# Kernel optimization log

Hardware: AMD Instinct MI355X
Metric: run time of the kernel (lower is better)

Reference implementation:

```python
import jax, jax.numpy as jnp
import numpy as np
from jax import lax

SCALE = 2
K_UP = 5
BN_EPS = 1e-5
DN = ('NCHW', 'OIHW', 'NCHW')


def bn_eval(x, gamma, beta):
    # BatchNorm2d in eval mode with running_mean=0, running_var=1
    s = gamma / jnp.sqrt(1.0 + BN_EPS)
    return x * s[None, :, None, None] + beta[None, :, None, None]


def pixel_shuffle(x, r):
    b, C, h, w = x.shape
    c = C // (r * r)
    x = x.reshape(b, c, r, r, h, w)
    x = x.transpose(0, 1, 4, 2, 5, 3)  # b, c, h, r, w, r
    return x.reshape(b, c, h * r, w * r)


def setup_inputs() -> dict:
    key = jax.random.key(0)
    ks = jax.random.split(key, 3)
    b, c, h, w = 4, 128, 64, 64
    c_mid = 64
    return {
        'X': jax.random.normal(ks[0], (b, c, h, w), dtype=jnp.float32),
        'comp_w': jax.random.normal(ks[1], (c_mid, c, 1, 1), dtype=jnp.float32) * 0.05,
        'comp_g': jnp.ones((c_mid,), jnp.float32),
        'comp_b': jnp.zeros((c_mid,), jnp.float32),
        'enc_w': jax.random.normal(ks[2], ((SCALE * K_UP) ** 2, c_mid, 3, 3), dtype=jnp.float32) * 0.05,
        'enc_g': jnp.ones(((SCALE * K_UP) ** 2,), jnp.float32),
        'enc_b': jnp.zeros(((SCALE * K_UP) ** 2,), jnp.float32),
    }


def reference(X, comp_w, comp_g, comp_b, enc_w, enc_g, enc_b):
    b, c, h, w = X.shape
    h_, w_ = h * SCALE, w * SCALE
    pad = K_UP // 2 * SCALE  # = 4

    # comp: 1x1 conv + BN + SiLU
    W = lax.conv_general_dilated(X, comp_w, (1, 1), [(0, 0), (0, 0)], dimension_numbers=DN)
    W = jax.nn.silu(bn_eval(W, comp_g, comp_b))
    # enc: 3x3 conv (pad 1) + BN, no activation
    W = lax.conv_general_dilated(W, enc_w, (1, 1), [(1, 1), (1, 1)], dimension_numbers=DN)
    W = bn_eval(W, enc_g, enc_b)
    # pixel shuffle -> [b, k_up^2, h_, w_], softmax over kernel dim
    W = pixel_shuffle(W, SCALE)
    W = jax.nn.softmax(W, axis=1)

    # nearest-neighbor upsample of X
    Xu = jnp.repeat(jnp.repeat(X, SCALE, axis=2), SCALE, axis=3)  # [b, c, h_, w_]
    # unfold: kernel k_up, dilation=scale, padding=pad (im2col, channel-major)
    P = lax.conv_general_dilated_patches(
        Xu, (K_UP, K_UP), (1, 1), [(pad, pad), (pad, pad)],
        rhs_dilation=(SCALE, SCALE), dimension_numbers=DN)  # [b, c*k^2, h_, w_]
    P = P.reshape(b, c, K_UP * K_UP, h_, w_)

    return jnp.einsum('bkhw,bckhw->bchw', W, P)
```

## Files before the change

### kernel.cpp

```cpp
#include <hip/hip_runtime.h>
#include <hip/hip_bf16.h>
#include <math.h>

#define Bn   4
#define CIN  128
#define Hh   64
#define Ww   64
#define HW   4096
#define CMID 64
#define KOC  100
#define H2   128
#define W2d  128
#define HW2  16384
#define KUP  5
#define BN_EPS 1e-5f
#define CCH  8

typedef __attribute__((ext_vector_type(4)))  short  short4v;
typedef __attribute__((ext_vector_type(8)))  short  short8v;
typedef __attribute__((ext_vector_type(16))) float  float16v;

__device__ __forceinline__ ushort f2bf(float v) {
    __hip_bfloat16 h = __float2bfloat16(v);
    return *(ushort*)&h;
}

__global__ __launch_bounds__(256) void comp_kernel(
    const float* __restrict__ X,
    const float* __restrict__ cw,
    const float* __restrict__ cg,
    const float* __restrict__ cb,
    const float* __restrict__ ew,
    unsigned* __restrict__ W1b,
    ushort* __restrict__ Abf)
{
    int tid = threadIdx.x;
    if (blockIdx.x < 288) {
        int i   = blockIdx.x * 256 + tid;
        int cm  = i & 63;
        int kop = (i >> 6) & 127;
        int tap = i >> 13;
        float v = (kop < KOC) ? ew[((size_t)(kop * CMID + cm)) * 9 + tap] : 0.f;
        Abf[i] = f2bf(v);
    }

    int gt  = blockIdx.x * 256 + tid;
    int pg  = gt & 1023;
    int cog = (gt >> 10) & 31;
    int b   = gt >> 15;
    int pix = pg * 4;
    int co0 = cog * 2;

    const float* xb = X + (size_t)b * CIN * HW + pix;
    float4 acc0 = make_float4(0.f, 0.f, 0.f, 0.f);
    float4 acc1 = make_float4(0.f, 0.f, 0.f, 0.f);

#pragma unroll 4
    for (int ci = 0; ci < CIN; ++ci) {
        float4 xv = *(const float4*)(xb + (size_t)ci * HW);
        float w0 = cw[(size_t)co0 * CIN + ci];
        float w1 = cw[(size_t)(co0 + 1) * CIN + ci];
        acc0.x += xv.x * w0; acc0.y += xv.y * w0; acc0.z += xv.z * w0; acc0.w += xv.w * w0;
        acc1.x += xv.x * w1; acc1.y += xv.y * w1; acc1.z += xv.z * w1; acc1.w += xv.w * w1;
    }

    float inv_s = rsqrtf(1.0f + BN_EPS);
    float s0 = cg[co0] * inv_s,     bb0 = cb[co0];
    float s1 = cg[co0 + 1] * inv_s, bb1 = cb[co0 + 1];
    float r0[4] = {acc0.x, acc0.y, acc0.z, acc0.w};
    float r1[4] = {acc1.x, acc1.y, acc1.z, acc1.w};
#pragma unroll
    for (int i = 0; i < 4; ++i) {
        float v0 = r0[i] * s0 + bb0; v0 = v0 / (1.f + expf(-v0));
        float v1 = r1[i] * s1 + bb1; v1 = v1 / (1.f + expf(-v1));
        unsigned pk = (unsigned)f2bf(v0) | ((unsigned)f2bf(v1) << 16);
        W1b[((size_t)b * HW + pix + i) * 32 + cog] = pk;
    }
}

__global__ __launch_bounds__(256) void enc_kernel(
    const ushort* __restrict__ W1b_us,
    const ushort* __restrict__ Abf,
    float* __restrict__ W2)
{
    __shared__ ushort Bs[3 * 34 * 72];

    int bid   = blockIdx.x;
    int whalf = bid & 1;
    int h     = (bid >> 1) & 63;
    int b     = bid >> 7;
    int w0    = whalf * 32;
    int tid   = threadIdx.x;

    const unsigned* src  = (const unsigned*)W1b_us;
    unsigned*       dstu = (unsigned*)Bs;
    for (int i = tid; i < 3 * 34 * 32; i += 256) {
        int cp = i & 31;
        int t  = i >> 5;
        int wl = t % 34;
        int r  = t / 34;
        int gr = h - 1 + r, gw = w0 - 1 + wl;
        unsigned val = 0u;
        if ((unsigned)gr < 64u && (unsigned)gw < 64u)
            val = src[((size_t)b * HW + gr * 64 + gw) * 32 + cp];
        dstu[(r * 34 + wl) * 36 + cp] = val;
    }
    __syncthreads();

    int lane = tid & 63;
    int wid  = tid >> 6;
    int n    = lane & 31;
    int q    = lane >> 5;

    float16v acc;
#pragma unroll
    for (int i = 0; i < 16; ++i) acc[i] = 0.f;

    const ushort* Arow = Abf + ((size_t)(wid * 32 + n)) * 64 + q * 8;

#pragma unroll
    for (int tap = 0; tap < 9; ++tap) {
        int dy = tap / 3, dx = tap % 3;
        int bbase = ((dy * 34) + n + dx) * 72 + q * 8;
        const ushort* Atap = Arow + (size_t)tap * 128 * 64;
#pragma unroll
        for (int c = 0; c < 4; ++c) {
            short8v a = *(const short8v*)(Atap + c * 16);
            short8v bf = *(const short8v*)(Bs + bbase + c * 16);
            acc = __builtin_amdgcn_mfma_f32_32x32x16_bf16(a, bf, acc, 0, 0, 0);
        }
    }

    int pixn = h * 64 + w0 + n;
    float* Wp = W2 + (size_t)b * KOC * HW + pixn;
#pragma unroll
    for (int reg = 0; reg < 16; ++reg) {
        int row = (reg & 3) + 8 * (reg >> 2) + 4 * q;
        int ko  = wid * 32 + row;
        if (ko < KOC) Wp[(size_t)ko * HW] = acc[reg];
    }
}

__global__ __launch_bounds__(256) void softmax_kernel(
    const float* __restrict__ W2,
    float* __restrict__ Wsm,
    const float* __restrict__ eg,
    const float* __restrict__ eb)
{
    int idx = blockIdx.x * blockDim.x + threadIdx.x;
    int pix = idx & (HW - 1);
    int sub = (idx >> 12) & 3;
    int b   = idx >> 14;

    float inv_s = rsqrtf(1.0f + BN_EPS);
    const float* pi = W2  + (size_t)b * KOC * HW + pix;
    float*       po = Wsm + (size_t)b * KOC * HW + pix;
    float v[25];
    float m = -1e30f;
#pragma unroll
    for (int k = 0; k < 25; ++k) {
        int ko = 4 * k + sub;
        v[k] = pi[(size_t)ko * HW] * (eg[ko] * inv_s) + eb[ko];
        m = fmaxf(m, v[k]);
    }
    float sum = 0.f;
#pragma unroll
    for (int k = 0; k < 25; ++k) {
        v[k] = expf(v[k] - m);
        sum += v[k];
    }
    float inv = 1.f / sum;
#pragma unroll
    for (int k = 0; k < 25; ++k)
        po[(size_t)(4 * k + sub) * HW] = v[k] * inv;
}

__global__ __launch_bounds__(256) void carafe_kernel(
    const float* __restrict__ X,
    const float* __restrict__ Wsm,
    float* __restrict__ out)
{
    int gt = blockIdx.x * blockDim.x + threadIdx.x;
    int w  = gt & 63;
    int h  = (gt >> 6) & 63;
    int b  = (gt >> 12) & 3;
    int chunk = gt >> 14;
    int c0 = chunk * CCH;
    int pix = h * Ww + w;

    float wt[100];
    const float* wpb = Wsm + (size_t)b * KOC * HW + pix;
#pragma unroll
    for (int k = 0; k < 25; ++k) {
        wt[k]      = wpb[(size_t)(4 * k + 0) * HW];
        wt[25 + k] = wpb[(size_t)(4 * k + 1) * HW];
        wt[50 + k] = wpb[(size_t)(4 * k + 2) * HW];
        wt[75 + k] = wpb[(size_t)(4 * k + 3) * HW];
    }

    int off[25];
#pragma unroll
    for (int ki = 0; ki < 5; ++ki) {
#pragma unroll
        for (int kj = 0; kj < 5; ++kj) {
            int k = ki * 5 + kj;
            int r = h + ki - 2, cc = w + kj - 2;
            bool valid = ((unsigned)r < 64u) && ((unsigned)cc < 64u);
            int rc = r < 0 ? 0 : (r > 63 ? 63 : r);
            int cx = cc < 0 ? 0 : (cc > 63 ? 63 : cc);
            off[k] = rc * Ww + cx;
            if (!valid) { wt[k] = 0.f; wt[25+k] = 0.f; wt[50+k] = 0.f; wt[75+k] = 0.f; }
        }
    }

    const float* xp = X + ((size_t)b * CIN + c0) * HW;
    float* o0 = out + ((size_t)b * CIN + c0) * HW2 + (2 * h) * W2d + 2 * w;

    for (int c = 0; c < CCH; ++c) {
        float x[25];
#pragma unroll
        for (int k = 0; k < 25; ++k) x[k] = xp[off[k]];
        float a0 = 0.f, a1 = 0.f, a2 = 0.f, a3 = 0.f;
#pragma unroll
        for (int k = 0; k < 25; ++k) {
            float xv = x[k];
            a0 += wt[k]      * xv;
            a1 += wt[25 + k] * xv;
            a2 += wt[50 + k] * xv;
            a3 += wt[75 + k] * xv;
        }
        *(float2*)o0          = make_float2(a0, a1);
        *(float2*)(o0 + W2d)  = make_float2(a2, a3);
        xp += HW;
        o0 += HW2;
    }
}

extern "C" void kernel_launch(void* const* d_in, const int* in_sizes, int n_in,
                              void* d_out, int out_size, void* d_ws, size_t ws_size,
                              hipStream_t stream)
{
    const float* X  = (const float*)d_in[0];
    const float* cw = (const float*)d_in[1];
    const float* cg = (const float*)d_in[2];
    const float* cb = (const float*)d_in[3];
    const float* ew = (const float*)d_in[4];
    const float* eg = (const float*)d_in[5];
    const float* eb = (const float*)d_in[6];
    float* out = (float*)d_out;

    char* ws = (char*)d_ws;
    unsigned* W1b = (unsigned*)ws;
    ushort*   Abf = (ushort*)(ws + 2097152);
    float*    W2  = (float*)(ws + 2097152 + 147456);
    float*    Wsm = W2 + (size_t)Bn * KOC * HW;

    comp_kernel   <<<512, 256, 0, stream>>>(X, cw, cg, cb, ew, W1b, Abf);
    enc_kernel    <<<512, 256, 0, stream>>>((const ushort*)W1b, Abf, W2);
    softmax_kernel<<<Bn * 4 * HW / 256, 256, 0, stream>>>(W2, Wsm, eg, eb);
    carafe_kernel <<<16 * Bn * HW / 256, 256, 0, stream>>>(X, Wsm, out);
}
```

Baseline: 129.4 us.

## Fuse BN and softmax into enc MFMA epilogue and restage comp weights in LDS

Moves the BN scale and the per-subpixel softmax into the enc kernel epilogue. Max and sum across the 100 output rows are reduced through shared memory across waves, so the separate softmax kernel and its extra write and read of the 100-channel map are removed. The comp kernel is remapped to one output channel per thread, with the 1x1 weights staged in padded LDS, writing bf16 directly. This doubles the comp grid, and every block reloads the full weight matrix into LDS.

```diff
diff --git a/kernel.cpp b/kernel.cpp
--- a/kernel.cpp
+++ b/kernel.cpp
@@ -31,59 +31,66 @@
     const float* __restrict__ cg,
     const float* __restrict__ cb,
     const float* __restrict__ ew,
-    unsigned* __restrict__ W1b,
+    ushort* __restrict__ W1b,
     ushort* __restrict__ Abf)
 {
+    __shared__ float cwS[64 * 129];
+
     int tid = threadIdx.x;
-    if (blockIdx.x < 288) {
-        int i   = blockIdx.x * 256 + tid;
+    int blk = blockIdx.x;
+
+    for (int i = tid; i < 64 * 128; i += 256) {
+        int co_s = i >> 7, ci_s = i & 127;
+        cwS[co_s * 129 + ci_s] = cw[i];
+    }
+
+    if (blk < 288) {
+        int i   = blk * 256 + tid;
         int cm  = i & 63;
         int kop = (i >> 6) & 127;
         int tap = i >> 13;
         float v = (kop < KOC) ? ew[((size_t)(kop * CMID + cm)) * 9 + tap] : 0.f;
         Abf[i] = f2bf(v);
     }
-
-    int gt  = blockIdx.x * 256 + tid;
-    int pg  = gt & 1023;
-    int cog = (gt >> 10) & 31;
-    int b   = gt >> 15;
-    int pix = pg * 4;
-    int co0 = cog * 2;
+    __syncthreads();
+
+    int b   = blk >> 8;
+    int pix = ((blk & 255) << 4) + ((tid >> 6) << 2);
+    int co  = tid & 63;
 
     const float* xb = X + (size_t)b * CIN * HW + pix;
-    float4 acc0 = make_float4(0.f, 0.f, 0.f, 0.f);
-    float4 acc1 = make_float4(0.f, 0.f, 0.f, 0.f);
+    const float* wrow = cwS + co * 129;
+    float a0 = 0.f, a1 = 0.f, a2 = 0.f, a3 = 0.f;
 
 #pragma unroll 4
     for (int ci = 0; ci < CIN; ++ci) {
         float4 xv = *(const float4*)(xb + (size_t)ci * HW);
-        float w0 = cw[(size_t)co0 * CIN + ci];
-        float w1 = cw[(size_t)(co0 + 1) * CIN + ci];
-        acc0.x += xv.x * w0; acc0.y += xv.y * w0; acc0.z += xv.z * w0; acc0.w += xv.w * w0;
-        acc1.x += xv.x * w1; acc1.y += xv.y * w1; acc1.z += xv.z * w1; acc1.w += xv.w * w1;
+        float w = wrow[ci];
+        a0 += xv.x * w; a1 += xv.y * w; a2 += xv.z * w; a3 += xv.w * w;
     }
 
     float inv_s = rsqrtf(1.0f + BN_EPS);
-    float s0 = cg[co0] * inv_s,     bb0 = cb[co0];
-    float s1 = cg[co0 + 1] * inv_s, bb1 = cb[co0 + 1];
-    float r0[4] = {acc0.x, acc0.y, acc0.z, acc0.w};
-    float r1[4] = {acc1.x, acc1.y, acc1.z, acc1.w};
+    float s0 = cg[co] * inv_s, bb0 = cb[co];
+    float r[4] = {a0, a1, a2, a3};
+    ushort* wp = W1b + ((size_t)b * HW + pix) * 64 + co;
 #pragma unroll
     for (int i = 0; i < 4; ++i) {
-        float v0 = r0[i] * s0 + bb0; v0 = v0 / (1.f + expf(-v0));
-        float v1 = r1[i] * s1 + bb1; v1 = v1 / (1.f + expf(-v1));
-        unsigned pk = (unsigned)f2bf(v0) | ((unsigned)f2bf(v1) << 16);
-        W1b[((size_t)b * HW + pix + i) * 32 + cog] = pk;
+        float v = r[i] * s0 + bb0;
+        v = v / (1.f + expf(-v));
+        wp[(size_t)i * 64] = f2bf(v);
     }
 }
 
 __global__ __launch_bounds__(256) void enc_kernel(
     const ushort* __restrict__ W1b_us,
     const ushort* __restrict__ Abf,
-    float* __restrict__ W2)
+    const float* __restrict__ eg,
+    const float* __restrict__ eb,
+    float* __restrict__ Wsm)
 {
     __shared__ ushort Bs[3 * 34 * 72];
+    __shared__ float  redm[4][8][32];
+    __shared__ float  reds[4][8][32];
 
     int bid   = blockIdx.x;
     int whalf = bid & 1;
@@ -131,48 +138,74 @@
         }
     }
 
+    float inv_s = rsqrtf(1.0f + BN_EPS);
+    int   widq  = wid * 2 + q;
+
+    float v[16];
+    float pmax[4] = {-1e30f, -1e30f, -1e30f, -1e30f};
+#pragma unroll
+    for (int g = 0; g < 4; ++g) {
+        int base = wid * 32 + 8 * g + 4 * q;
+        if (base < KOC) {
+            float4 gg = *(const float4*)(eg + base);
+            float4 bb = *(const float4*)(eb + base);
+            float v0 = acc[4*g+0] * (gg.x * inv_s) + bb.x;
+            float v1 = acc[4*g+1] * (gg.y * inv_s) + bb.y;
+            float v2 = acc[4*g+2] * (gg.z * inv_s) + bb.z;
+            float v3 = acc[4*g+3] * (gg.w * inv_s) + bb.w;
+            v[4*g+0] = v0; v[4*g+1] = v1; v[4*g+2] = v2; v[4*g+3] = v3;
+            pmax[0] = fmaxf(pmax[0], v0);
+            pmax[1] = fmaxf(pmax[1], v1);
+            pmax[2] = fmaxf(pmax[2], v2);
+            pmax[3] = fmaxf(pmax[3], v3);
+        } else {
+            v[4*g+0] = -1e30f; v[4*g+1] = -1e30f;
+            v[4*g+2] = -1e30f; v[4*g+3] = -1e30f;
+        }
+    }
+
+#pragma unroll
+    for (int j = 0; j < 4; ++j) redm[j][widq][n] = pmax[j];
+    __syncthreads();
+    float m[4];
+#pragma unroll
+    for (int j = 0; j < 4; ++j) {
+        float mm = redm[j][0][n];
+#pragma unroll
+        for (int i = 1; i < 8; ++i) mm = fmaxf(mm, redm[j][i][n]);
+        m[j] = mm;
+    }
+
+    float psum[4] = {0.f, 0.f, 0.f, 0.f};
+#pragma unroll
+    for (int g = 0; g < 4; ++g) {
+#pragma unroll
+        for (int j = 0; j < 4; ++j) {
+            float e = expf(v[4*g+j] - m[j]);
+            v[4*g+j] = e;
+            psum[j] += e;
+        }
+    }
+#pragma unroll
+    for (int j = 0; j < 4; ++j) reds[j][widq][n] = psum[j];
+    __syncthreads();
+    float inv[4];
+#pragma unroll
+    for (int j = 0; j < 4; ++j) {
+        float ss = reds[j][0][n];
+#pragma unroll
+        for (int i = 1; i < 8; ++i) ss += reds[j][i][n];
+        inv[j] = 1.f / ss;
+    }
+
     int pixn = h * 64 + w0 + n;
-    float* Wp = W2 + (size_t)b * KOC * HW + pixn;
+    float* Wp = Wsm + (size_t)b * KOC * HW + pixn;
 #pragma unroll
     for (int reg = 0; reg < 16; ++reg) {
         int row = (reg & 3) + 8 * (reg >> 2) + 4 * q;
         int ko  = wid * 32 + row;
-        if (ko < KOC) Wp[(size_t)ko * HW] = acc[reg];
-    }
-}
-
-__global__ __launch_bounds__(256) void softmax_kernel(
-    const float* __restrict__ W2,
-    float* __restrict__ Wsm,
-    const float* __restrict__ eg,
-    const float* __restrict__ eb)
-{
-    int idx = blockIdx.x * blockDim.x + threadIdx.x;
-    int pix = idx & (HW - 1);
-    int sub = (idx >> 12) & 3;
-    int b   = idx >> 14;
-
-    float inv_s = rsqrtf(1.0f + BN_EPS);
-    const float* pi = W2  + (size_t)b * KOC * HW + pix;
-    float*       po = Wsm + (size_t)b * KOC * HW + pix;
-    float v[25];
-    float m = -1e30f;
-#pragma unroll
-    for (int k = 0; k < 25; ++k) {
-        int ko = 4 * k + sub;
-        v[k] = pi[(size_t)ko * HW] * (eg[ko] * inv_s) + eb[ko];
-        m = fmaxf(m, v[k]);
-    }
-    float sum = 0.f;
-#pragma unroll
-    for (int k = 0; k < 25; ++k) {
-        v[k] = expf(v[k] - m);
-        sum += v[k];
-    }
-    float inv = 1.f / sum;
-#pragma unroll
-    for (int k = 0; k < 25; ++k)
-        po[(size_t)(4 * k + sub) * HW] = v[k] * inv;
+        if (ko < KOC) Wp[(size_t)ko * HW] = v[reg] * inv[reg & 3];
+    }
 }
 
 __global__ __launch_bounds__(256) void carafe_kernel(
@@ -250,13 +283,11 @@
     float* out = (float*)d_out;
 
     char* ws = (char*)d_ws;
-    unsigned* W1b = (unsigned*)ws;
-    ushort*   Abf = (ushort*)(ws + 2097152);
-    float*    W2  = (float*)(ws + 2097152 + 147456);
-    float*    Wsm = W2 + (size_t)Bn * KOC * HW;
-
-    comp_kernel   <<<512, 256, 0, stream>>>(X, cw, cg, cb, ew, W1b, Abf);
-    enc_kernel    <<<512, 256, 0, stream>>>((const ushort*)W1b, Abf, W2);
-    softmax_kernel<<<Bn * 4 * HW / 256, 256, 0, stream>>>(W2, Wsm, eg, eb);
-    carafe_kernel <<<16 * Bn * HW / 256, 256, 0, stream>>>(X, Wsm, out);
-}
+    ushort* W1b = (ushort*)ws;
+    ushort* Abf = (ushort*)(ws + 2097152);
+    float*  Wsm = (float*)(ws + 2097152 + 147456);
+
+    comp_kernel  <<<1024, 256, 0, stream>>>(X, cw, cg, cb, ew, W1b, Abf);
+    enc_kernel   <<<512, 256, 0, stream>>>(W1b, Abf, eg, eb, Wsm);
+    carafe_kernel<<<16 * Bn * HW / 256, 256, 0, stream>>>(X, Wsm, out);
+}
```

Result: no change. 128.1 us (-1.0%).
